# Performance work log

Measured on AMD Instinct MI355X. Metric: run time of the kernel, lower is better.

The kernel has to match this reference:

```python
import jax, jax.numpy as jnp
import numpy as np

K = 7      # kernel_size
PAD = 3    # padding ('same' with stride 1)
G = 16     # groups


def _unfold(x):
    """torch nn.Unfold equivalent, stride=1, dilation=1.
    Returns [B, C, K*K, H, W] with kernel positions ordered (kh, kw),
    matching torch's (c, kh, kw) channel-major layout after reshape."""
    B, C, H, W = x.shape
    xp = jnp.pad(x, ((0, 0), (0, 0), (PAD, PAD), (PAD, PAD)))
    patches = jnp.stack(
        [xp[:, :, i:i + H, j:j + W] for i in range(K) for j in range(K)],
        axis=2,
    )
    return patches


def setup_inputs() -> dict:
    key = jax.random.key(0)
    k1, k2, k3 = jax.random.split(key, 3)
    B, C, H, W = 4, 256, 64, 64
    x = jax.random.normal(k1, (B, C, H, W), dtype=jnp.float32)
    # 1x1 conv producing kernel_prod*groups = 49*16 = 784 channels (with bias)
    w_kernel = jax.random.normal(k2, (G * K * K, C), dtype=jnp.float32) * 0.05
    b_kernel = jax.random.normal(k3, (G * K * K,), dtype=jnp.float32) * 0.05
    return {"x": x, "w_kernel": w_kernel, "b_kernel": b_kernel}


def reference(x, w_kernel, b_kernel):
    B, C, H, W = x.shape
    Cg = C // G
    # unfolded input: [B, G, C//G, K*K, H, W]
    patches = _unfold(x).reshape(B, G, Cg, K * K, H, W)
    # dynamic per-pixel kernel: AvgPool(k=1) is identity at stride 1,
    # then 1x1 conv with bias -> [B, G*K*K, H, W]
    kern = jnp.einsum('bchw,kc->bkhw', x, w_kernel) + b_kernel[None, :, None, None]
    kern = kern.reshape(B, G, 1, K * K, H, W)
    # multiply and sum-reduce over kernel positions, flatten groups
    out = (patches * kern).sum(axis=3).reshape(B, C, H, W)
    return out
```

## Files before the change

kernel.cpp:

```cpp
#include <hip/hip_runtime.h>


#define B_   4
#define C_   256
#define G_   16
#define KK_  49
#define KS_  7
#define PD_  3

#define XP8_BYTES (B_*32*4096*8*2)
#define WBF_OFF   XP8_BYTES

#define SKW   28
#define HC_   70
#define HPOS  (10*HC_)

typedef __attribute__((ext_vector_type(8))) short bf16x8;
typedef __attribute__((ext_vector_type(4))) float f32x4;
typedef unsigned short ushort_t;

__device__ inline unsigned f2bf(float f) {
    unsigned u = __float_as_uint(f);
    u += 0x7FFF + ((u >> 16) & 1);
    return u >> 16;
}

__global__ __launch_bounds__(256)
void cvt_xp8(const float* __restrict__ x, const float* __restrict__ wk,
             ushort_t* __restrict__ xp8, unsigned* __restrict__ wbf) {
    const int t = threadIdx.x;
    if (blockIdx.x == 64) {
        const int slice = blockIdx.z * 4 + blockIdx.y;
        const float2* wk2 = (const float2*)wk;
        const int base = slice * 6272;
        for (int k = t; k < 6272; k += 256) {
            float2 v = wk2[base + k];
            wbf[base + k] = f2bf(v.x) | (f2bf(v.y) << 16);
        }
        return;
    }
    __shared__ float tile[64][65];
    const int p0 = blockIdx.x * 64;
    const int c0 = blockIdx.y * 64;
    const int b  = blockIdx.z;
    const int px_r = t & 63;
    #pragma unroll
    for (int i = 0; i < 16; ++i) {
        int ch = (t >> 6) + i * 4;
        tile[ch][px_r] = x[((size_t)(b * C_ + c0 + ch) << 12) + p0 + px_r];
    }
    __syncthreads();
    const int px = t & 63;
    const int ob = t >> 6;
    #pragma unroll
    for (int jj = 0; jj < 2; ++jj) {
        const int j = ob + jj * 4;
        unsigned u[4];
        #pragma unroll
        for (int k2 = 0; k2 < 4; ++k2) {
            float a0 = tile[j * 8 + 2 * k2][px];
            float a1 = tile[j * 8 + 2 * k2 + 1][px];
            u[k2] = f2bf(a0) | (f2bf(a1) << 16);
        }
        ushort_t* dst = xp8 + (((size_t)((b << 5) + (c0 >> 3) + j) << 12) + p0 + px) * 8;
        *(uint4*)dst = make_uint4(u[0], u[1], u[2], u[3]);
    }
}

__device__ inline uint4 stage_ld(const ushort_t* __restrict__ xp8,
                                 int b, int oct, int gy0, int e) {
    const int row = e / HC_;
    const int col = e - row * HC_;
    const int sy = gy0 + row - PD_;
    const int sx = col - PD_;
    if (sy >= 0 && sy < 64 && sx >= 0 && sx < 64)
        return *(const uint4*)(xp8 + (((size_t)((b << 5) + oct) << 12) + sy * 64 + sx) * 8);
    return make_uint4(0u, 0u, 0u, 0u);
}

__global__ __launch_bounds__(256, 4)
void inv_fused(const ushort_t* __restrict__ xp8,
               const ushort_t* __restrict__ wbf,
               const float* __restrict__ bk,
               float* __restrict__ out) {
    __shared__ unsigned kern2[256 * SKW];
    __shared__ unsigned halo4[HPOS * 4];

    const int bid  = blockIdx.x;
    const int g    = bid >> 6;
    const int b    = (bid >> 4) & 3;
    const int tile = bid & 15;
    const int gy0  = tile * 4;
    const int p0   = tile * 256;

    const int tid  = threadIdx.x;
    const int wv   = tid >> 6;
    const int ln15 = tid & 15;
    const int quad = (tid & 63) >> 4;

    f32x4 acc[16];
    #pragma unroll
    for (int i = 0; i < 16; ++i) acc[i] = (f32x4){0.f, 0.f, 0.f, 0.f};

    const ushort_t* ap[4];
    #pragma unroll
    for (int mt = 0; mt < 4; ++mt) {
        int r = mt * 16 + ln15; if (r > KK_ - 1) r = KK_ - 1;
        ap[mt] = wbf + (size_t)(g * KK_ + r) * C_ + quad * 8;
    }
    const ushort_t* bp = xp8 + (((size_t)((b << 5) + quad) << 12) + p0 + wv * 64 + ln15) * 8;

    bf16x8 af[3][4], bf[3][4];
    #pragma unroll
    for (int kb = 0; kb < 2; ++kb) {
        const int cc = kb * 32;
        #pragma unroll
        for (int mt = 0; mt < 4; ++mt)
            af[kb][mt] = *(const bf16x8*)(ap[mt] + cc);
        #pragma unroll
        for (int nt = 0; nt < 4; ++nt)
            bf[kb][nt] = *(const bf16x8*)(bp + ((size_t)cc << 12) + nt * 128);
    }

    #pragma unroll
    for (int k = 0; k < 8; ++k) {
        const int cur = k % 3;
        if (k < 6) {
            const int nxt = (k + 2) % 3;
            const int cc  = (k + 2) * 32;
            #pragma unroll
            for (int mt = 0; mt < 4; ++mt)
                af[nxt][mt] = *(const bf16x8*)(ap[mt] + cc);
            #pragma unroll
            for (int nt = 0; nt < 4; ++nt)
                bf[nxt][nt] = *(const bf16x8*)(bp + ((size_t)cc << 12) + nt * 128);
        }
        #pragma unroll
        for (int mt = 0; mt < 4; ++mt) {
            #pragma unroll
            for (int nt = 0; nt < 4; ++nt) {
                acc[mt * 4 + nt] = __builtin_amdgcn_mfma_f32_16x16x32_bf16(
                    af[cur][mt], bf[cur][nt], acc[mt * 4 + nt], 0, 0, 0);
            }
        }
    }

    for (int e = tid; e < HPOS; e += 256)
        *(uint4*)&halo4[e * 4] = stage_ld(xp8, b, 2 * g, gy0, e);

    #pragma unroll
    for (int mt = 0; mt < 3; ++mt) {
        const int m0 = mt * 16 + quad * 4;
        const float b0 = bk[g * KK_ + m0],     b1 = bk[g * KK_ + m0 + 1];
        const float b2 = bk[g * KK_ + m0 + 2], b3 = bk[g * KK_ + m0 + 3];
        #pragma unroll
        for (int nt = 0; nt < 4; ++nt) {
            const int p = wv * 64 + nt * 16 + ln15;
            uint2 d;
            d.x = f2bf(acc[mt * 4 + nt][0] + b0) | (f2bf(acc[mt * 4 + nt][1] + b1) << 16);
            d.y = f2bf(acc[mt * 4 + nt][2] + b2) | (f2bf(acc[mt * 4 + nt][3] + b3) << 16);
            *(uint2*)&kern2[p * SKW + mt * 8 + quad * 2] = d;
        }
    }
    if (quad == 0) {
        const float b48 = bk[g * KK_ + 48];
        #pragma unroll
        for (int nt = 0; nt < 4; ++nt) {
            const int p = wv * 64 + nt * 16 + ln15;
            kern2[p * SKW + 24] = f2bf(acc[12 + nt][0] + b48);
        }
    }
    __syncthreads();

    float kv[KK_];
    {
        const uint4* kr = (const uint4*)&kern2[tid * SKW];
        unsigned kd[28];
        #pragma unroll
        for (int q = 0; q < 7; ++q) {
            uint4 h = kr[q];
            kd[4*q] = h.x; kd[4*q+1] = h.y; kd[4*q+2] = h.z; kd[4*q+3] = h.w;
        }
        #pragma unroll
        for (int k = 0; k < KK_; ++k) {
            unsigned d = kd[k >> 1];
            kv[k] = __uint_as_float((k & 1) ? (d & 0xffff0000u) : (d << 16));
        }
    }

    uint4 pf0 = stage_ld(xp8, b, 2 * g + 1, gy0, tid);
    uint4 pf1 = stage_ld(xp8, b, 2 * g + 1, gy0, tid + 256);
    uint4 pf2 = (tid < HPOS - 512) ? stage_ld(xp8, b, 2 * g + 1, gy0, tid + 512)
                                   : make_uint4(0u, 0u, 0u, 0u);

    const int py = tid >> 6, px = tid & 63;

    #pragma unroll 1
    for (int hb = 0; hb < 2; ++hb) {
        if (hb) {
            __syncthreads();
            *(uint4*)&halo4[tid * 4] = pf0;
            *(uint4*)&halo4[(tid + 256) * 4] = pf1;
            if (tid < HPOS - 512) *(uint4*)&halo4[(tid + 512) * 4] = pf2;
            __syncthreads();
        }
        float a[8];
        #pragma unroll
        for (int q = 0; q < 8; ++q) a[q] = 0.f;
        #pragma unroll
        for (int kh = 0; kh < KS_; ++kh) {
            const uint4* hr = (const uint4*)&halo4[((py + kh) * HC_ + px) * 4];
            #pragma unroll
            for (int kw = 0; kw < KS_; ++kw) {
                uint4 hv = hr[kw];
                float kk = kv[kh * KS_ + kw];
                a[0] = fmaf(__uint_as_float(hv.x << 16), kk, a[0]);
                a[1] = fmaf(__uint_as_float(hv.x),       kk, a[1]);
                a[2] = fmaf(__uint_as_float(hv.y << 16), kk, a[2]);
                a[3] = fmaf(__uint_as_float(hv.y),       kk, a[3]);
                a[4] = fmaf(__uint_as_float(hv.z << 16), kk, a[4]);
                a[5] = fmaf(__uint_as_float(hv.z),       kk, a[5]);
                a[6] = fmaf(__uint_as_float(hv.w << 16), kk, a[6]);
                a[7] = fmaf(__uint_as_float(hv.w),       kk, a[7]);
            }
        }
        const size_t o = ((size_t)(b * C_ + g * 16 + hb * 8) << 12) + p0 + tid;
        #pragma unroll
        for (int q = 0; q < 8; ++q)
            out[o + ((size_t)q << 12)] = a[q];
    }
}

extern "C" void kernel_launch(void* const* d_in, const int* in_sizes, int n_in,
                              void* d_out, int out_size, void* d_ws, size_t ws_size,
                              hipStream_t stream) {
    const float* x  = (const float*)d_in[0];
    const float* wk = (const float*)d_in[1];
    const float* bk = (const float*)d_in[2];
    float* o = (float*)d_out;

    ushort_t* xp8 = (ushort_t*)d_ws;
    unsigned* wbf = (unsigned*)((char*)d_ws + WBF_OFF);

    cvt_xp8<<<dim3(65, 4, B_), dim3(256), 0, stream>>>(x, wk, xp8, wbf);
    inv_fused<<<dim3(1024), dim3(256), 0, stream>>>(
        xp8, (const ushort_t*)wbf, bk, o);
}
```

Before: 104.0 us.

## Pre-pad bf16 input in global memory and read conv taps directly

The bf16 channel-octet buffer now uses a zero-padded 70x70 spatial layout, cleared with a memset each call and filled in its interior by the conversion kernel. The fused kernel drops the LDS halo staging, its bounds-checked loads and the associated barriers, and reads the 49 taps straight from global memory, relying on the L1/L2 caches for reuse. The goal is to remove staging overhead and synchronisation, and to raise occupancy by freeing LDS. In exchange every call pays an extra multi-megabyte memset, and tap reads move from LDS to the vector cache, which has less bandwidth.

```diff
diff --git a/kernel.cpp b/kernel.cpp
--- a/kernel.cpp
+++ b/kernel.cpp
@@ -8,12 +8,12 @@
 #define KS_  7
 #define PD_  3
 
-#define XP8_BYTES (B_*32*4096*8*2)
+#define PR_   70
+#define OCTS  (PR_*PR_)
+#define XP8_BYTES (B_*32*OCTS*8*2)
 #define WBF_OFF   XP8_BYTES
 
 #define SKW   28
-#define HC_   70
-#define HPOS  (10*HC_)
 
 typedef __attribute__((ext_vector_type(8))) short bf16x8;
 typedef __attribute__((ext_vector_type(4))) float f32x4;
@@ -40,14 +40,14 @@
         return;
     }
     __shared__ float tile[64][65];
-    const int p0 = blockIdx.x * 64;
-    const int c0 = blockIdx.y * 64;
-    const int b  = blockIdx.z;
+    const int row = blockIdx.x;
+    const int c0  = blockIdx.y * 64;
+    const int b   = blockIdx.z;
     const int px_r = t & 63;
     #pragma unroll
     for (int i = 0; i < 16; ++i) {
         int ch = (t >> 6) + i * 4;
-        tile[ch][px_r] = x[((size_t)(b * C_ + c0 + ch) << 12) + p0 + px_r];
+        tile[ch][px_r] = x[((size_t)(b * C_ + c0 + ch) << 12) + row * 64 + px_r];
     }
     __syncthreads();
     const int px = t & 63;
@@ -62,20 +62,10 @@
             float a1 = tile[j * 8 + 2 * k2 + 1][px];
             u[k2] = f2bf(a0) | (f2bf(a1) << 16);
         }
-        ushort_t* dst = xp8 + (((size_t)((b << 5) + (c0 >> 3) + j) << 12) + p0 + px) * 8;
+        ushort_t* dst = xp8 + ((size_t)((b << 5) + (c0 >> 3) + j) * OCTS
+                               + (row + PD_) * PR_ + PD_ + px) * 8;
         *(uint4*)dst = make_uint4(u[0], u[1], u[2], u[3]);
     }
-}
-
-__device__ inline uint4 stage_ld(const ushort_t* __restrict__ xp8,
-                                 int b, int oct, int gy0, int e) {
-    const int row = e / HC_;
-    const int col = e - row * HC_;
-    const int sy = gy0 + row - PD_;
-    const int sx = col - PD_;
-    if (sy >= 0 && sy < 64 && sx >= 0 && sx < 64)
-        return *(const uint4*)(xp8 + (((size_t)((b << 5) + oct) << 12) + sy * 64 + sx) * 8);
-    return make_uint4(0u, 0u, 0u, 0u);
 }
 
 __global__ __launch_bounds__(256, 4)
@@ -84,7 +74,6 @@
                const float* __restrict__ bk,
                float* __restrict__ out) {
     __shared__ unsigned kern2[256 * SKW];
-    __shared__ unsigned halo4[HPOS * 4];
 
     const int bid  = blockIdx.x;
     const int g    = bid >> 6;
@@ -108,18 +97,18 @@
         int r = mt * 16 + ln15; if (r > KK_ - 1) r = KK_ - 1;
         ap[mt] = wbf + (size_t)(g * KK_ + r) * C_ + quad * 8;
     }
-    const ushort_t* bp = xp8 + (((size_t)((b << 5) + quad) << 12) + p0 + wv * 64 + ln15) * 8;
+    const ushort_t* bp = xp8 + ((size_t)((b << 5) + quad) * OCTS
+                                + (gy0 + wv + PD_) * PR_ + PD_ + ln15) * 8;
 
     bf16x8 af[3][4], bf[3][4];
     #pragma unroll
     for (int kb = 0; kb < 2; ++kb) {
-        const int cc = kb * 32;
         #pragma unroll
         for (int mt = 0; mt < 4; ++mt)
-            af[kb][mt] = *(const bf16x8*)(ap[mt] + cc);
+            af[kb][mt] = *(const bf16x8*)(ap[mt] + kb * 32);
         #pragma unroll
         for (int nt = 0; nt < 4; ++nt)
-            bf[kb][nt] = *(const bf16x8*)(bp + ((size_t)cc << 12) + nt * 128);
+            bf[kb][nt] = *(const bf16x8*)(bp + (size_t)kb * 4 * OCTS * 8 + nt * 128);
     }
 
     #pragma unroll
@@ -127,13 +116,12 @@
         const int cur = k % 3;
         if (k < 6) {
             const int nxt = (k + 2) % 3;
-            const int cc  = (k + 2) * 32;
             #pragma unroll
             for (int mt = 0; mt < 4; ++mt)
-                af[nxt][mt] = *(const bf16x8*)(ap[mt] + cc);
+                af[nxt][mt] = *(const bf16x8*)(ap[mt] + (k + 2) * 32);
             #pragma unroll
             for (int nt = 0; nt < 4; ++nt)
-                bf[nxt][nt] = *(const bf16x8*)(bp + ((size_t)cc << 12) + nt * 128);
+                bf[nxt][nt] = *(const bf16x8*)(bp + (size_t)(k + 2) * 4 * OCTS * 8 + nt * 128);
         }
         #pragma unroll
         for (int mt = 0; mt < 4; ++mt) {
@@ -144,9 +132,6 @@
             }
         }
     }
-
-    for (int e = tid; e < HPOS; e += 256)
-        *(uint4*)&halo4[e * 4] = stage_ld(xp8, b, 2 * g, gy0, e);
 
     #pragma unroll
     for (int mt = 0; mt < 3; ++mt) {
@@ -170,7 +155,6 @@
             kern2[p * SKW + 24] = f2bf(acc[12 + nt][0] + b48);
         }
     }
-    __syncthreads();
 
     float kv[KK_];
     {
@@ -188,31 +172,19 @@
         }
     }
 
-    uint4 pf0 = stage_ld(xp8, b, 2 * g + 1, gy0, tid);
-    uint4 pf1 = stage_ld(xp8, b, 2 * g + 1, gy0, tid + 256);
-    uint4 pf2 = (tid < HPOS - 512) ? stage_ld(xp8, b, 2 * g + 1, gy0, tid + 512)
-                                   : make_uint4(0u, 0u, 0u, 0u);
-
     const int py = tid >> 6, px = tid & 63;
-
     #pragma unroll 1
     for (int hb = 0; hb < 2; ++hb) {
-        if (hb) {
-            __syncthreads();
-            *(uint4*)&halo4[tid * 4] = pf0;
-            *(uint4*)&halo4[(tid + 256) * 4] = pf1;
-            if (tid < HPOS - 512) *(uint4*)&halo4[(tid + 512) * 4] = pf2;
-            __syncthreads();
-        }
+        const ushort_t* tapb = xp8 + ((size_t)((b << 5) + 2 * g + hb) * OCTS
+                                      + (gy0 + py) * PR_ + px) * 8;
         float a[8];
         #pragma unroll
         for (int q = 0; q < 8; ++q) a[q] = 0.f;
         #pragma unroll
         for (int kh = 0; kh < KS_; ++kh) {
-            const uint4* hr = (const uint4*)&halo4[((py + kh) * HC_ + px) * 4];
             #pragma unroll
             for (int kw = 0; kw < KS_; ++kw) {
-                uint4 hv = hr[kw];
+                uint4 hv = *(const uint4*)(tapb + (kh * PR_ + kw) * 8);
                 float kk = kv[kh * KS_ + kw];
                 a[0] = fmaf(__uint_as_float(hv.x << 16), kk, a[0]);
                 a[1] = fmaf(__uint_as_float(hv.x),       kk, a[1]);
@@ -242,6 +214,7 @@
     ushort_t* xp8 = (ushort_t*)d_ws;
     unsigned* wbf = (unsigned*)((char*)d_ws + WBF_OFF);
 
+    hipMemsetAsync(xp8, 0, XP8_BYTES, stream);
     cvt_xp8<<<dim3(65, 4, B_), dim3(256), 0, stream>>>(x, wk, xp8, wbf);
     inv_fused<<<dim3(1024), dim3(256), 0, stream>>>(
         xp8, (const ushort_t*)wbf, bk, o);
```

After: 109.5 us. +5.2%, slower.
